# Optimization experiments

Hardware: AMD Instinct MI355X
Metric: run time of the kernel (lower is better)

## Reference

```python
import jax, jax.numpy as jnp
import numpy as np

N_NODES = 100000
N_EDGES = 1600000
D_IN = 128
D_HID = 128
D_OUT = 128


def _sage_conv(x, src, dst, W_l, b_l, W_r, num_nodes):
    # PyG SAGEConv (aggr='mean'): out = lin_l(mean_{j in N(i)} x_j) + lin_r(x_i)
    msg = x[src]  # [E, d] gather source features
    agg = jax.ops.segment_sum(msg, dst, num_segments=num_nodes)  # [N, d]
    deg = jax.ops.segment_sum(jnp.ones((src.shape[0],), x.dtype), dst, num_segments=num_nodes)
    mean = agg / jnp.maximum(deg, 1.0)[:, None]
    return mean @ W_l.T + b_l + x @ W_r.T


def setup_inputs() -> dict:
    key = jax.random.key(0)
    ks = jax.random.split(key, 8)
    x = jax.random.normal(ks[0], (N_NODES, D_IN), dtype=jnp.float32)
    edge_index = jax.random.randint(ks[1], (2, N_EDGES), 0, N_NODES, dtype=jnp.int64)
    s = 1.0 / np.sqrt(D_IN)
    W_l1 = jax.random.uniform(ks[2], (D_HID, D_IN), jnp.float32, -s, s)
    b_l1 = jnp.zeros((D_HID,), jnp.float32)
    W_r1 = jax.random.uniform(ks[3], (D_HID, D_IN), jnp.float32, -s, s)
    s2 = 1.0 / np.sqrt(D_HID)
    W_l2 = jax.random.uniform(ks[4], (D_OUT, D_HID), jnp.float32, -s2, s2)
    b_l2 = jnp.zeros((D_OUT,), jnp.float32)
    W_r2 = jax.random.uniform(ks[5], (D_OUT, D_HID), jnp.float32, -s2, s2)
    return {"x": x, "edge_index": edge_index, "W_l1": W_l1, "b_l1": b_l1,
            "W_r1": W_r1, "W_l2": W_l2, "b_l2": b_l2, "W_r2": W_r2}


def reference(x, edge_index, W_l1, b_l1, W_r1, W_l2, b_l2, W_r2):
    src, dst = edge_index[0], edge_index[1]
    n = x.shape[0]
    h = _sage_conv(x, src, dst, W_l1, b_l1, W_r1, n)
    h = jax.nn.relu(h)
    out = _sage_conv(h, src, dst, W_l2, b_l2, W_r2, n)
    return out
```

## Files before the change

### kernel.cpp

```cpp
#include <hip/hip_runtime.h>
#include <stdint.h>

typedef short bf16x8 __attribute__((ext_vector_type(8)));
typedef unsigned short u16x8 __attribute__((ext_vector_type(8)));
typedef float f32x4 __attribute__((ext_vector_type(4)));

#define NPB 512
#define BSHIFT 9
#define MAXBUCK 256
#define STAGE_CAP 12288
#define LROW 136
#define BINWIN 2048

__device__ __forceinline__ short f2bf(float f) {
    uint32_t u = __float_as_uint(f);
    u += 0x7fffu + ((u >> 16) & 1u);
    return (short)(u >> 16);
}
__device__ __forceinline__ float bf2f(unsigned short s) {
    return __uint_as_float((uint32_t)s << 16);
}

__global__ __launch_bounds__(256) void prep_kernel(
    const float* __restrict__ x, short* __restrict__ xb, int nx,
    const float* __restrict__ w0, const float* __restrict__ w1,
    const float* __restrict__ w2, const float* __restrict__ w3,
    short* __restrict__ o0, short* __restrict__ o1,
    short* __restrict__ o2, short* __restrict__ o3,
    const int* __restrict__ dst, int* __restrict__ bcnt, int E, int B,
    int cxBlocks, int histBlocks)
{
    int b = blockIdx.x;
    if (b < cxBlocks) {
        int i = (b * 256 + threadIdx.x) * 8;
        if (i + 8 <= nx) {
            const float4 v0 = *(const float4*)(x + i);
            const float4 v1 = *(const float4*)(x + i + 4);
            bf16x8 o;
            o[0] = f2bf(v0.x); o[1] = f2bf(v0.y); o[2] = f2bf(v0.z); o[3] = f2bf(v0.w);
            o[4] = f2bf(v1.x); o[5] = f2bf(v1.y); o[6] = f2bf(v1.z); o[7] = f2bf(v1.w);
            *(bf16x8*)(xb + i) = o;
        } else {
            for (int j = i; j < nx; ++j) xb[j] = f2bf(x[j]);
        }
        return;
    }
    b -= cxBlocks;
    if (b < 64) {
        int i = b * 256 + threadIdx.x;
        o0[i] = f2bf(w0[i]);
        o1[i] = f2bf(w1[i]);
        o2[i] = f2bf(w2[i]);
        o3[i] = f2bf(w3[i]);
        return;
    }
    b -= 64;
    __shared__ int h[MAXBUCK];
    for (int i = threadIdx.x; i < B; i += 256) h[i] = 0;
    __syncthreads();
    const int stride = histBlocks * 256;
    for (int e = b * 256 + threadIdx.x; e < E; e += stride)
        atomicAdd(&h[dst[e] >> BSHIFT], 1);
    __syncthreads();
    for (int i = threadIdx.x; i < B; i += 256)
        if (h[i]) atomicAdd(&bcnt[i], h[i]);
}

__global__ __launch_bounds__(256) void bscan_kernel(const int* __restrict__ bcnt,
                                                    int* __restrict__ bbase,
                                                    int* __restrict__ gcur,
                                                    int* __restrict__ rowptr,
                                                    int E, int N, int B) {
    __shared__ int s[256];
    int t = threadIdx.x;
    int v = (t < B) ? bcnt[t] : 0;
    s[t] = v;
    __syncthreads();
    for (int off = 1; off < 256; off <<= 1) {
        int a = (t >= off) ? s[t - off] : 0;
        __syncthreads();
        s[t] += a;
        __syncthreads();
    }
    int excl = s[t] - v;
    if (t < B) { bbase[t] = excl; gcur[t] = excl; }
    if (t == B - 1) bbase[B] = excl + v;
    if (t == 0) rowptr[N] = E;
}

__global__ __launch_bounds__(256) void bin_kernel(const int* __restrict__ src,
                                                  const int* __restrict__ dst,
                                                  int* __restrict__ gcur,
                                                  unsigned int* __restrict__ binned,
                                                  int E, int B) {
    __shared__ int cnt[MAXBUCK];
    __shared__ int base[MAXBUCK];
    for (int i = threadIdx.x; i < B; i += 256) cnt[i] = 0;
    __syncthreads();
    const int e0 = blockIdx.x * BINWIN;
    const int eEnd = (e0 + BINWIN < E) ? (e0 + BINWIN) : E;
#pragma unroll 4
    for (int e = e0 + threadIdx.x; e < eEnd; e += 256)
        atomicAdd(&cnt[dst[e] >> BSHIFT], 1);
    __syncthreads();
    for (int i = threadIdx.x; i < B; i += 256) {
        int c = cnt[i];
        base[i] = c ? atomicAdd(&gcur[i], c) : 0;
        cnt[i] = 0;
    }
    __syncthreads();
#pragma unroll 4
    for (int e = e0 + threadIdx.x; e < eEnd; e += 256) {
        int sv = src[e], dv = dst[e];
        int b = dv >> BSHIFT;
        int off = atomicAdd(&cnt[b], 1);
        binned[base[b] + off] = ((unsigned)sv << BSHIFT) | (unsigned)(dv & (NPB - 1));
    }
}

__global__ __launch_bounds__(256) void build_kernel(const unsigned int* __restrict__ binned,
                                                    const int* __restrict__ bbase,
                                                    int* __restrict__ rowptr,
                                                    int* __restrict__ csr, int N) {
    __shared__ int hist[NPB];
    __shared__ int cur[NPB];
    __shared__ int scanb[256];
    __shared__ int stage[STAGE_CAP];
    const int b = blockIdx.x;
    const int t = threadIdx.x;
    const int cbeg = bbase[b], cend = bbase[b + 1];
    const int cnt = cend - cbeg;
    for (int i = t; i < NPB; i += 256) hist[i] = 0;
    __syncthreads();
    for (int i = t; i < cnt; i += 256)
        atomicAdd(&hist[binned[cbeg + i] & (NPB - 1)], 1);
    __syncthreads();
    const int h0 = hist[2 * t], h1 = hist[2 * t + 1];
    const int ps = h0 + h1;
    scanb[t] = ps;
    __syncthreads();
    for (int off = 1; off < 256; off <<= 1) {
        int a = (t >= off) ? scanb[t - off] : 0;
        __syncthreads();
        scanb[t] += a;
        __syncthreads();
    }
    const int e0 = scanb[t] - ps;
    cur[2 * t]     = e0;
    cur[2 * t + 1] = e0 + h0;
    __syncthreads();
    const int node0 = b << BSHIFT;
    for (int i = t; i < NPB; i += 256) {
        int node = node0 + i;
        if (node < N) rowptr[node] = cbeg + cur[i];
    }
    __syncthreads();
    for (int i = t; i < cnt; i += 256) {
        unsigned rec = binned[cbeg + i];
        int ld  = rec & (NPB - 1);
        int pos = atomicAdd(&cur[ld], 1);
        if (pos < STAGE_CAP) stage[pos] = (int)(rec >> BSHIFT);
        else                 csr[cbeg + pos] = (int)(rec >> BSHIFT);
    }
    __syncthreads();
    const int lim = cnt < STAGE_CAP ? cnt : STAGE_CAP;
    for (int i = t; i < lim; i += 256)
        csr[cbeg + i] = stage[i];
}

#define ACC8(u) do { \
    a0 += bf2f(u[0]); a1 += bf2f(u[1]); a2 += bf2f(u[2]); a3 += bf2f(u[3]); \
    a4 += bf2f(u[4]); a5 += bf2f(u[5]); a6 += bf2f(u[6]); a7 += bf2f(u[7]); } while (0)

template <bool RELU>
__global__ __launch_bounds__(256) void fused_kernel(
    const short* __restrict__ feat, const int* __restrict__ csr,
    const int* __restrict__ rowptr,
    const short* __restrict__ Wl, const short* __restrict__ Wr,
    const float* __restrict__ bias,
    short* __restrict__ outb, float* __restrict__ outf, int N)
{
    __shared__ short lmean[32 * LROW];
    const int lane = threadIdx.x & 63;
    const int wave = threadIdx.x >> 6;
    const int q    = lane >> 4;
    const int ql   = lane & 15;
    const int nb0  = blockIdx.x * 32;
    const int m0w  = nb0 + wave * 8;

    for (int it = 0; it < 2; ++it) {
        const int node = m0w + it * 4 + q;
        const int lrow = wave * 8 + it * 4 + q;
        float a0=0,a1=0,a2=0,a3=0,a4=0,a5=0,a6=0,a7=0;
        if (node < N) {
            const int beg = rowptr[node], end = rowptr[node + 1];
            int e = beg;
            for (; e + 4 <= end; e += 4) {
                const int s0 = csr[e], s1 = csr[e+1], s2 = csr[e+2], s3 = csr[e+3];
                const u16x8 u0 = *(const u16x8*)(feat + (size_t)s0 * 128 + ql * 8);
                const u16x8 u1 = *(const u16x8*)(feat + (size_t)s1 * 128 + ql * 8);
                const u16x8 u2 = *(const u16x8*)(feat + (size_t)s2 * 128 + ql * 8);
                const u16x8 u3 = *(const u16x8*)(feat + (size_t)s3 * 128 + ql * 8);
                ACC8(u0); ACC8(u1); ACC8(u2); ACC8(u3);
            }
            for (; e < end; ++e) {
                const u16x8 u = *(const u16x8*)(feat + (size_t)csr[e] * 128 + ql * 8);
                ACC8(u);
            }
            const float r = 1.0f / fmaxf((float)(end - beg), 1.0f);
            bf16x8 o;
            o[0] = f2bf(a0 * r); o[1] = f2bf(a1 * r); o[2] = f2bf(a2 * r); o[3] = f2bf(a3 * r);
            o[4] = f2bf(a4 * r); o[5] = f2bf(a5 * r); o[6] = f2bf(a6 * r); o[7] = f2bf(a7 * r);
            *(bf16x8*)(lmean + (size_t)lrow * LROW + ql * 8) = o;
        } else {
            *(bf16x8*)(lmean + (size_t)lrow * LROW + ql * 8) = (bf16x8)0;
        }
    }
    __syncthreads();

    const int t2 = wave >> 1;
    const int h  = wave & 1;
    const int m0 = nb0 + t2 * 16;
    f32x4 acc[4];
#pragma unroll
    for (int i = 0; i < 4; ++i) acc[i] = (f32x4)0.0f;
    const bool valid = (m0 + ql < N);

#pragma unroll
    for (int kk = 0; kk < 4; ++kk) {
        const int kb = kk * 32 + q * 8;
        const bf16x8 a = *(const bf16x8*)(lmean + (size_t)(t2 * 16 + ql) * LROW + kb);
#pragma unroll
        for (int nt = 0; nt < 4; ++nt) {
            const bf16x8 b = *(const bf16x8*)(Wl + (size_t)(h * 64 + nt * 16 + ql) * 128 + kb);
            acc[nt] = __builtin_amdgcn_mfma_f32_16x16x32_bf16(a, b, acc[nt], 0, 0, 0);
        }
    }
#pragma unroll
    for (int kk = 0; kk < 4; ++kk) {
        const int kb = kk * 32 + q * 8;
        bf16x8 a = (bf16x8)0;
        if (valid) a = *(const bf16x8*)(feat + (size_t)(m0 + ql) * 128 + kb);
#pragma unroll
        for (int nt = 0; nt < 4; ++nt) {
            const bf16x8 b = *(const bf16x8*)(Wr + (size_t)(h * 64 + nt * 16 + ql) * 128 + kb);
            acc[nt] = __builtin_amdgcn_mfma_f32_16x16x32_bf16(a, b, acc[nt], 0, 0, 0);
        }
    }

    const int rbase = m0 + q * 4;
#pragma unroll
    for (int nt = 0; nt < 4; ++nt) {
        const int col = h * 64 + nt * 16 + ql;
        const float bc = bias[col];
#pragma unroll
        for (int r = 0; r < 4; ++r) {
            const int node = rbase + r;
            if (node < N) {
                float v = acc[nt][r] + bc;
                if (RELU) outb[(size_t)node * 128 + col] = f2bf(fmaxf(v, 0.0f));
                else      outf[(size_t)node * 128 + col] = v;
            }
        }
    }
}

extern "C" void kernel_launch(void* const* d_in, const int* in_sizes, int n_in,
                              void* d_out, int out_size, void* d_ws, size_t ws_size,
                              hipStream_t stream) {
    const float* x   = (const float*)d_in[0];
    const int*   ei  = (const int*)d_in[1];
    const float* Wl1 = (const float*)d_in[2];
    const float* bl1 = (const float*)d_in[3];
    const float* Wr1 = (const float*)d_in[4];
    const float* Wl2 = (const float*)d_in[5];
    const float* bl2 = (const float*)d_in[6];
    const float* Wr2 = (const float*)d_in[7];

    const int N = in_sizes[0] / 128;
    const int E = in_sizes[1] / 2;
    const int* src = ei;
    const int* dst = ei + E;
    const int B = (N + NPB - 1) >> BSHIFT;

    char* wsb = (char*)d_ws;
    short* hbuf = (short*)wsb;
    size_t off = (size_t)N * 128 * 2;
    short* wl1 = (short*)(wsb + off); off += 16384 * 2;
    short* wr1 = (short*)(wsb + off); off += 16384 * 2;
    short* wl2 = (short*)(wsb + off); off += 16384 * 2;
    short* wr2 = (short*)(wsb + off); off += 16384 * 2;
    int* rowptr = (int*)(wsb + off);
    off += ((size_t)(N + 1) * 4 + 15) & ~(size_t)15;
    int* csr = (int*)(wsb + off);
    off += ((size_t)E * 4 + 15) & ~(size_t)15;
    unsigned int* binned = (unsigned int*)(wsb + off);
    off += ((size_t)E * 4 + 15) & ~(size_t)15;
    int* bcnt  = (int*)(wsb + off);
    int* bbase = bcnt + (MAXBUCK + 1);
    int* gcur  = bbase + (MAXBUCK + 1);

    short* xb  = (short*)d_out;
    float* out = (float*)d_out;

    const int nx = N * 128;
    const int cxBlocks    = (nx / 8 + 255) / 256;
    const int histBlocks  = 1024;
    const int fusedBlocks = (N + 31) / 32;
    const int binBlocks   = (E + BINWIN - 1) / BINWIN;

    (void)hipMemsetAsync(bcnt, 0, (size_t)(MAXBUCK + 1) * sizeof(int), stream);

    prep_kernel<<<cxBlocks + 64 + histBlocks, 256, 0, stream>>>(
        x, xb, nx, Wl1, Wr1, Wl2, Wr2, wl1, wr1, wl2, wr2,
        dst, bcnt, E, B, cxBlocks, histBlocks);
    bscan_kernel<<<1, 256, 0, stream>>>(bcnt, bbase, gcur, rowptr, E, N, B);
    bin_kernel<<<binBlocks, 256, 0, stream>>>(src, dst, gcur, binned, E, B);
    build_kernel<<<B, 256, 0, stream>>>(binned, bbase, rowptr, csr, N);

    fused_kernel<true><<<fusedBlocks, 256, 0, stream>>>(xb, csr, rowptr, wl1, wr1, bl1,
                                                        hbuf, (float*)nullptr, N);
    fused_kernel<false><<<fusedBlocks, 256, 0, stream>>>(hbuf, csr, rowptr, wl2, wr2, bl2,
                                                         (short*)nullptr, out, N);
}
```

Before: 442.1 us.

## Make fused SAGE kernel persistent with per-wave atomic tile scheduling

```diff
diff --git a/kernel.cpp b/kernel.cpp
--- a/kernel.cpp
+++ b/kernel.cpp
@@ -10,7 +10,7 @@
 #define MAXBUCK 256
 #define STAGE_CAP 12288
 #define LROW 136
-#define BINWIN 2048
+#define BINWIN 4096
 
 __device__ __forceinline__ short f2bf(float f) {
     uint32_t u = __float_as_uint(f);
@@ -178,88 +178,90 @@
     const int* __restrict__ rowptr,
     const short* __restrict__ Wl, const short* __restrict__ Wr,
     const float* __restrict__ bias,
-    short* __restrict__ outb, float* __restrict__ outf, int N)
+    short* __restrict__ outb, float* __restrict__ outf,
+    int* __restrict__ ctr, int N)
 {
-    __shared__ short lmean[32 * LROW];
+    __shared__ short lmean[64 * LROW];
     const int lane = threadIdx.x & 63;
     const int wave = threadIdx.x >> 6;
     const int q    = lane >> 4;
     const int ql   = lane & 15;
-    const int nb0  = blockIdx.x * 32;
-    const int m0w  = nb0 + wave * 8;
-
-    for (int it = 0; it < 2; ++it) {
-        const int node = m0w + it * 4 + q;
-        const int lrow = wave * 8 + it * 4 + q;
-        float a0=0,a1=0,a2=0,a3=0,a4=0,a5=0,a6=0,a7=0;
-        if (node < N) {
-            const int beg = rowptr[node], end = rowptr[node + 1];
-            int e = beg;
-            for (; e + 4 <= end; e += 4) {
-                const int s0 = csr[e], s1 = csr[e+1], s2 = csr[e+2], s3 = csr[e+3];
-                const u16x8 u0 = *(const u16x8*)(feat + (size_t)s0 * 128 + ql * 8);
-                const u16x8 u1 = *(const u16x8*)(feat + (size_t)s1 * 128 + ql * 8);
-                const u16x8 u2 = *(const u16x8*)(feat + (size_t)s2 * 128 + ql * 8);
-                const u16x8 u3 = *(const u16x8*)(feat + (size_t)s3 * 128 + ql * 8);
-                ACC8(u0); ACC8(u1); ACC8(u2); ACC8(u3);
+    short* lw = lmean + (size_t)wave * 16 * LROW;
+    const int nTiles = (N + 15) >> 4;
+
+    for (;;) {
+        int tile = 0;
+        if (lane == 0) tile = atomicAdd(ctr, 1);
+        tile = __shfl(tile, 0);
+        if (tile >= nTiles) break;
+        const int m0 = tile * 16;
+
+        for (int it = 0; it < 4; ++it) {
+            const int node = m0 + it * 4 + q;
+            float a0=0,a1=0,a2=0,a3=0,a4=0,a5=0,a6=0,a7=0;
+            if (node < N) {
+                const int beg = rowptr[node], end = rowptr[node + 1];
+                int e = beg;
+                for (; e + 4 <= end; e += 4) {
+                    const int s0 = csr[e], s1 = csr[e+1], s2 = csr[e+2], s3 = csr[e+3];
+                    const u16x8 u0 = *(const u16x8*)(feat + (size_t)s0 * 128 + ql * 8);
+                    const u16x8 u1 = *(const u16x8*)(feat + (size_t)s1 * 128 + ql * 8);
+                    const u16x8 u2 = *(const u16x8*)(feat + (size_t)s2 * 128 + ql * 8);
+                    const u16x8 u3 = *(const u16x8*)(feat + (size_t)s3 * 128 + ql * 8);
+                    ACC8(u0); ACC8(u1); ACC8(u2); ACC8(u3);
+                }
+                for (; e < end; ++e) {
+                    const u16x8 u = *(const u16x8*)(feat + (size_t)csr[e] * 128 + ql * 8);
+                    ACC8(u);
+                }
+                const float r = 1.0f / fmaxf((float)(end - beg), 1.0f);
+                bf16x8 o;
+                o[0] = f2bf(a0 * r); o[1] = f2bf(a1 * r); o[2] = f2bf(a2 * r); o[3] = f2bf(a3 * r);
+                o[4] = f2bf(a4 * r); o[5] = f2bf(a5 * r); o[6] = f2bf(a6 * r); o[7] = f2bf(a7 * r);
+                *(bf16x8*)(lw + (size_t)(it * 4 + q) * LROW + ql * 8) = o;
             }
-            for (; e < end; ++e) {
-                const u16x8 u = *(const u16x8*)(feat + (size_t)csr[e] * 128 + ql * 8);
-                ACC8(u);
+        }
+
+        f32x4 acc[8];
+#pragma unroll
+        for (int i = 0; i < 8; ++i) acc[i] = (f32x4)0.0f;
+        const bool valid = (m0 + ql < N);
+
+#pragma unroll
+        for (int kk = 0; kk < 4; ++kk) {
+            const int kb = kk * 32 + q * 8;
+            const bf16x8 a = *(const bf16x8*)(lw + (size_t)ql * LROW + kb);
+#pragma unroll
+            for (int nt = 0; nt < 8; ++nt) {
+                const bf16x8 b = *(const bf16x8*)(Wl + (size_t)(nt * 16 + ql) * 128 + kb);
+                acc[nt] = __builtin_amdgcn_mfma_f32_16x16x32_bf16(a, b, acc[nt], 0, 0, 0);
             }
-            const float r = 1.0f / fmaxf((float)(end - beg), 1.0f);
-            bf16x8 o;
-            o[0] = f2bf(a0 * r); o[1] = f2bf(a1 * r); o[2] = f2bf(a2 * r); o[3] = f2bf(a3 * r);
-            o[4] = f2bf(a4 * r); o[5] = f2bf(a5 * r); o[6] = f2bf(a6 * r); o[7] = f2bf(a7 * r);
-            *(bf16x8*)(lmean + (size_t)lrow * LROW + ql * 8) = o;
-        } else {
-            *(bf16x8*)(lmean + (size_t)lrow * LROW + ql * 8) = (bf16x8)0;
-        }
-    }
-    __syncthreads();
-
-    const int t2 = wave >> 1;
-    const int h  = wave & 1;
-    const int m0 = nb0 + t2 * 16;
-    f32x4 acc[4];
-#pragma unroll
-    for (int i = 0; i < 4; ++i) acc[i] = (f32x4)0.0f;
-    const bool valid = (m0 + ql < N);
-
-#pragma unroll
-    for (int kk = 0; kk < 4; ++kk) {
-        const int kb = kk * 32 + q * 8;
-        const bf16x8 a = *(const bf16x8*)(lmean + (size_t)(t2 * 16 + ql) * LROW + kb);
-#pragma unroll
-        for (int nt = 0; nt < 4; ++nt) {
-            const bf16x8 b = *(const bf16x8*)(Wl + (size_t)(h * 64 + nt * 16 + ql) * 128 + kb);
-            acc[nt] = __builtin_amdgcn_mfma_f32_16x16x32_bf16(a, b, acc[nt], 0, 0, 0);
-        }
-    }
-#pragma unroll
-    for (int kk = 0; kk < 4; ++kk) {
-        const int kb = kk * 32 + q * 8;
-        bf16x8 a = (bf16x8)0;
-        if (valid) a = *(const bf16x8*)(feat + (size_t)(m0 + ql) * 128 + kb);
-#pragma unroll
-        for (int nt = 0; nt < 4; ++nt) {
-            const bf16x8 b = *(const bf16x8*)(Wr + (size_t)(h * 64 + nt * 16 + ql) * 128 + kb);
-            acc[nt] = __builtin_amdgcn_mfma_f32_16x16x32_bf16(a, b, acc[nt], 0, 0, 0);
-        }
-    }
-
-    const int rbase = m0 + q * 4;
-#pragma unroll
-    for (int nt = 0; nt < 4; ++nt) {
-        const int col = h * 64 + nt * 16 + ql;
-        const float bc = bias[col];
-#pragma unroll
-        for (int r = 0; r < 4; ++r) {
-            const int node = rbase + r;
-            if (node < N) {
-                float v = acc[nt][r] + bc;
-                if (RELU) outb[(size_t)node * 128 + col] = f2bf(fmaxf(v, 0.0f));
-                else      outf[(size_t)node * 128 + col] = v;
+        }
+#pragma unroll
+        for (int kk = 0; kk < 4; ++kk) {
+            const int kb = kk * 32 + q * 8;
+            bf16x8 a = (bf16x8)0;
+            if (valid) a = *(const bf16x8*)(feat + (size_t)(m0 + ql) * 128 + kb);
+#pragma unroll
+            for (int nt = 0; nt < 8; ++nt) {
+                const bf16x8 b = *(const bf16x8*)(Wr + (size_t)(nt * 16 + ql) * 128 + kb);
+                acc[nt] = __builtin_amdgcn_mfma_f32_16x16x32_bf16(a, b, acc[nt], 0, 0, 0);
+            }
+        }
+
+        const int rbase = m0 + q * 4;
+#pragma unroll
+        for (int nt = 0; nt < 8; ++nt) {
+            const int col = nt * 16 + ql;
+            const float bc = bias[col];
+#pragma unroll
+            for (int r = 0; r < 4; ++r) {
+                const int node = rbase + r;
+                if (node < N) {
+                    float v = acc[nt][r] + bc;
+                    if (RELU) outb[(size_t)node * 128 + col] = f2bf(fmaxf(v, 0.0f));
+                    else      outf[(size_t)node * 128 + col] = v;
+                }
             }
         }
     }
@@ -299,6 +301,7 @@
     int* bcnt  = (int*)(wsb + off);
     int* bbase = bcnt + (MAXBUCK + 1);
     int* gcur  = bbase + (MAXBUCK + 1);
+    int* ctr   = gcur + MAXBUCK;
 
     short* xb  = (short*)d_out;
     float* out = (float*)d_out;
@@ -306,10 +309,11 @@
     const int nx = N * 128;
     const int cxBlocks    = (nx / 8 + 255) / 256;
     const int histBlocks  = 1024;
-    const int fusedBlocks = (N + 31) / 32;
     const int binBlocks   = (E + BINWIN - 1) / BINWIN;
+    const int fusedBlocks = 2048;
 
     (void)hipMemsetAsync(bcnt, 0, (size_t)(MAXBUCK + 1) * sizeof(int), stream);
+    (void)hipMemsetAsync(ctr, 0, 2 * sizeof(int), stream);
 
     prep_kernel<<<cxBlocks + 64 + histBlocks, 256, 0, stream>>>(
         x, xb, nx, Wl1, Wr1, Wl2, Wr2, wl1, wr1, wl2, wr2,
@@ -319,7 +323,7 @@
     build_kernel<<<B, 256, 0, stream>>>(binned, bbase, rowptr, csr, N);
 
     fused_kernel<true><<<fusedBlocks, 256, 0, stream>>>(xb, csr, rowptr, wl1, wr1, bl1,
-                                                        hbuf, (float*)nullptr, N);
+                                                        hbuf, (float*)nullptr, ctr, N);
     fused_kernel<false><<<fusedBlocks, 256, 0, stream>>>(hbuf, csr, rowptr, wl2, wr2, bl2,
-                                                         (short*)nullptr, out, N);
-}
+                                                         (short*)nullptr, out, ctr + 1, N);
+}
```

Result: slower. 688.1 us (+55.6%).
